# Kernel optimization log

Measured on AMD Instinct MI355X. Metric: run time of the kernel, lower is better.

The kernel has to match this reference:

```python
import jax, jax.numpy as jnp
import numpy as np

B, T, C = 2, 2048, 1024
H, D, R = 16, 64, 32  # heads, head_dim, compression rank (R < D)


def setup_inputs() -> dict:
    key = jax.random.key(0)
    ks = jax.random.split(key, 8)
    s = 0.02
    return {
        "hidden_states": jax.random.normal(ks[0], (B, T, C), jnp.float32),
        "c_attn_w": jax.random.normal(ks[1], (C, 3 * C), jnp.float32) * s,
        "c_attn_b": jnp.zeros((3 * C,), jnp.float32),
        "c_proj_w": jax.random.normal(ks[2], (C, C), jnp.float32) * s,
        "c_proj_b": jnp.zeros((C,), jnp.float32),
        "wk_c": jax.random.normal(ks[3], (D, R), jnp.float32) * (1.0 / np.sqrt(D)),
        "wk_e": jax.random.normal(ks[4], (R, D), jnp.float32) * (1.0 / np.sqrt(R)),
        "wv_c": jax.random.normal(ks[5], (D, R), jnp.float32) * (1.0 / np.sqrt(D)),
        "wv_e": jax.random.normal(ks[6], (R, D), jnp.float32) * (1.0 / np.sqrt(R)),
    }


def reference(hidden_states, c_attn_w, c_attn_b, c_proj_w, c_proj_b,
              wk_c, wk_e, wv_c, wv_e):
    b, t, c = hidden_states.shape
    # GPT2 Conv1D: x @ W + b, then split into Q, K, V
    qkv = hidden_states @ c_attn_w + c_attn_b  # [B,T,3C]
    q, k, v = jnp.split(qkv, 3, axis=-1)

    def split_heads(x):  # [B,T,C] -> [B,H,T,D]
        return x.reshape(b, t, H, D).transpose(0, 2, 1, 3)

    q = split_heads(q)
    k = split_heads(k)
    v = split_heads(v)

    # Low-rank KV compression then expansion (rank R < D path)
    k_lat = jnp.einsum('bhtd,dr->bhtr', k, wk_c)  # [B,H,T,R]
    v_lat = jnp.einsum('bhtd,dr->bhtr', v, wv_c)
    k_exp = jnp.einsum('bhtr,rd->bhtd', k_lat, wk_e)  # [B,H,T,D]
    v_exp = jnp.einsum('bhtr,rd->bhtd', v_lat, wv_e)

    # Causal SDPA (attention_mask is None and q_len > 1 -> is_causal=True)
    scale = 1.0 / np.sqrt(D).astype(np.float32)
    scores = jnp.einsum('bhqd,bhkd->bhqk', q, k_exp) * scale  # [B,H,T,T]
    causal = jnp.tril(jnp.ones((t, t), dtype=bool))
    scores = jnp.where(causal[None, None], scores, jnp.finfo(scores.dtype).min)
    probs = jax.nn.softmax(scores, axis=-1)
    attn = jnp.einsum('bhqk,bhkd->bhqd', probs, v_exp)  # [B,H,T,D]

    # Merge heads and output projection
    attn = attn.transpose(0, 2, 1, 3).reshape(b, t, c)
    out = attn @ c_proj_w + c_proj_b
    return out
```

## Files before the change

### kernel.cpp

```cpp
#include <hip/hip_runtime.h>
#include <cstddef>

typedef __attribute__((ext_vector_type(8))) __bf16 bf16x8;
typedef __attribute__((ext_vector_type(4))) float f32x4;
typedef unsigned short u16;
typedef unsigned int   u32;

#define SCLF (0.125f * 1.44269504f)

__device__ __forceinline__ u16 f2bf(float f){
  union { float f; u32 u; } v; v.f = f;
  u32 r = v.u + 0x7FFFu + ((v.u >> 16) & 1u);
  return (u16)(r >> 16);
}
__device__ __forceinline__ u32 cvtpk(float lo, float hi){
  u32 r; asm("v_cvt_pk_bf16_f32 %0, %1, %2" : "=v"(r) : "v"(lo), "v"(hi)); return r;
}
__device__ __forceinline__ void gll16(const void* g, void* l){
  __builtin_amdgcn_global_load_lds((__attribute__((address_space(1))) void*)g,
                                   (__attribute__((address_space(3))) void*)l, 16, 0, 0);
}

__global__ __launch_bounds__(256) void convert_all(const float* __restrict__ x,
      const float* __restrict__ Wa, const float* __restrict__ ba, const float* __restrict__ Wp,
      const float* __restrict__ kc, const float* __restrict__ ke,
      const float* __restrict__ vc, const float* __restrict__ ve,
      u16* __restrict__ Xb, u16* __restrict__ Wab, u16* __restrict__ Mb,
      float* __restrict__ b2, u16* __restrict__ WpTb){
  __shared__ float SH[4160];
  const int bid = blockIdx.x, tid = threadIdx.x;
  if (bid < 4096){
    int i = bid*256 + tid;
    float4 v = ((const float4*)x)[i];
    uint2 r; r.x = cvtpk(v.x, v.y); r.y = cvtpk(v.z, v.w);
    ((uint2*)Xb)[i] = r;
  } else if (bid < 7168){
    int i = (bid-4096)*256 + tid;
    float4 v = ((const float4*)Wa)[i];
    uint2 r; r.x = cvtpk(v.x, v.y); r.y = cvtpk(v.z, v.w);
    ((uint2*)Wab)[i] = r;
  } else if (bid == 7168){
    #pragma unroll
    for (int t=0;t<8;++t){
      int idx = t*256 + tid;
      Mb[idx] = f2bf(ke[idx]*SCLF);
      int d = idx>>5, r = idx&31;
      Mb[2048 + r*64 + d] = f2bf(kc[idx]);
      Mb[4096 + r*64 + d] = f2bf(vc[idx]);
      Mb[6144 + idx] = f2bf(ve[idx]);
    }
  } else if (bid < 7172){
    const int part = bid - 7169;
    float* BaL = SH;
    float* W65 = SH + 1024;
    *(float4*)&BaL[tid*4] = *(const float4*)&ba[part*1024 + tid*4];
    {
      const float* msrc = (part==0) ? ke : (part==1) ? kc : vc;
      #pragma unroll
      for (int i=0;i<8;++i){
        int idx = tid + i*256;
        float v = msrc[idx];
        int r, d;
        if (part == 0){ r = idx >> 6; d = idx & 63; }
        else          { d = idx >> 5; r = idx & 31; }
        W65[r*65 + d] = v;
      }
    }
    __syncthreads();
    const float scl = (part==0) ? SCLF : 1.f;
    #pragma unroll
    for (int t=0;t<2;++t){
      int l = tid + t*256;
      int hh = l >> 5, r = l & 31;
      float acc = 0.f;
      for (int d=0;d<64;++d) acc += BaL[hh*64 + d] * W65[r*65 + d];
      b2[part*512 + l] = acc * scl;
    }
  } else {
    const int idx2 = bid - 7172;
    const int c0 = (idx2 & 15)*64, n0 = (idx2 >> 4)*64;
    float* tile = SH;
    int tx = tid & 63, ty = tid >> 6;
    #pragma unroll 4
    for (int k=0;k<16;++k){
      int r = 4*k + ty;
      tile[r*65 + tx] = Wp[(size_t)(c0+r)*1024 + n0 + tx];
    }
    __syncthreads();
    #pragma unroll 4
    for (int k=0;k<16;++k){
      int r = 4*k + ty;
      WpTb[(size_t)(n0+r)*1024 + c0 + tx] = f2bf(tile[tx*65 + r]);
    }
  }
}

__global__ __launch_bounds__(256) void fold_gemms(const u16* __restrict__ Wab,
      const u16* __restrict__ Mb, const u16* __restrict__ WpTb,
      u16* __restrict__ Wt, u16* __restrict__ W2t){
  __shared__ u16 As[4096];
  __shared__ u16 Bs[2048];
  const int cc = blockIdx.x, y = blockIdx.y;
  const int tid = threadIdx.x, wv = tid>>6, ln = tid&63;
  const int lr = ln&15, g8 = (ln>>4)*8, gq = ln>>4;
  const int c0 = cc*64;
  const int lrow = ln>>3, lcol = ((ln&7) ^ lrow)*8;
  const int swz = (lr&7)*8;
  const bool qkv = (y < 48);
  const int ph = qkv ? y : (y - 48);
  const u16* A = qkv ? (Wab + (size_t)c0*3072 + ph*64) : (WpTb + (size_t)c0*1024 + ph*64);
  const u16* B = qkv ? (Mb + (ph>>4)*2048) : (Mb + 6144);
  const size_t astr = qkv ? 3072 : 1024;
  #pragma unroll
  for (int it=0;it<3;++it){
    int c3 = wv*3 + it;
    if (c3 < 8) gll16(A + (size_t)(c3*8+lrow)*astr + lcol, &As[c3*512]);
    else { int bc = c3-8; gll16(B + (bc*8+lrow)*64 + lcol, &Bs[bc*512]); }
  }
  __syncthreads();
  f32x4 acc[2] = {};
  const int wr = (wv>>1)*32, wn = wv&1;
  #pragma unroll
  for (int ks=0;ks<2;++ks){
    int off = (ks*32 + g8) ^ swz;
    bf16x8 bf = *(const bf16x8*)&Bs[(wn*16+lr)*64 + off];
    #pragma unroll
    for (int mt=0;mt<2;++mt){
      bf16x8 af = *(const bf16x8*)&As[(wr+mt*16+lr)*64 + off];
      acc[mt] = __builtin_amdgcn_mfma_f32_16x16x32_bf16(af, bf, acc[mt], 0,0,0);
    }
  }
  if (qkv){
    const int n = (ph>>4)*512 + (ph&15)*32 + wn*16 + lr;
    #pragma unroll
    for (int mt=0;mt<2;++mt){
      union { u16 s[4]; uint2 v; } pk;
      #pragma unroll
      for (int r=0;r<4;++r) pk.s[r] = f2bf(acc[mt][r]);
      *(uint2*)&Wt[(size_t)n*1024 + c0 + wr + mt*16 + 4*gq] = pk.v;
    }
  } else {
    const int col = ph*32 + wn*16 + lr;
    #pragma unroll
    for (int mt=0;mt<2;++mt)
      #pragma unroll
      for (int r=0;r<4;++r)
        W2t[(size_t)(c0 + wr + mt*16 + 4*gq + r)*512 + col] = f2bf(acc[mt][r]);
  }
}

template<typename OT>
__global__ __launch_bounds__(256) void gemm64(const u16* __restrict__ A, const u16* __restrict__ Bt,
        const float* __restrict__ bias, OT* __restrict__ C, u16* __restrict__ Vt,
        int M, int N, int K, int ldc){
  __shared__ u16 As[64*64];
  __shared__ u16 Bs[128*64];
  const int nwg = gridDim.x * gridDim.y;
  const int id  = blockIdx.x + gridDim.x * blockIdx.y;
  const int nid = (id & 7) * (nwg >> 3) + (id >> 3);
  const int bx = nid % gridDim.x, by = nid / gridDim.x;
  const int tid = threadIdx.x, wv = tid>>6, ln = tid&63;
  const int lr = ln&15, g8 = (ln>>4)*8;
  const int m0 = bx*64, n0 = by*128;
  const int wr = (wv>>1)*32, wc = (wv&1)*64;
  const int lrow = ln>>3, lcol = ((ln&7) ^ lrow)*8;
  const int swz = (lr&7)*8;
  f32x4 acc[2][4] = {};
  const int nk = K >> 6;
  for (int kt=0; kt<nk; ++kt){
    #pragma unroll
    for (int it=0; it<6; ++it){
      int chunk = wv*6 + it;
      if (chunk < 8){
        int row = chunk*8 + lrow;
        gll16(A + (size_t)(m0+row)*K + kt*64 + lcol, &As[chunk*512]);
      } else {
        int bc = chunk - 8;
        int row = bc*8 + lrow;
        gll16(Bt + (size_t)(n0+row)*K + kt*64 + lcol, &Bs[bc*512]);
      }
    }
    __syncthreads();
    #pragma unroll
    for (int ks=0; ks<2; ++ks){
      int off = (ks*32 + g8) ^ swz;
      bf16x8 af[2], bfr[4];
      #pragma unroll
      for (int mt=0;mt<2;++mt) af[mt]  = *(const bf16x8*)&As[(wr+mt*16+lr)*64 + off];
      #pragma unroll
      for (int nt=0;nt<4;++nt) bfr[nt] = *(const bf16x8*)&Bs[(wc+nt*16+lr)*64 + off];
      #pragma unroll
      for (int mt=0;mt<2;++mt)
        #pragma unroll
        for (int nt=0;nt<4;++nt)
          acc[mt][nt] = __builtin_amdgcn_mfma_f32_16x16x32_bf16(af[mt], bfr[nt], acc[mt][nt], 0,0,0);
    }
    __syncthreads();
  }
  if (Vt && n0 >= 1024){
    #pragma unroll
    for (int mt=0;mt<2;++mt){
      int row0 = m0 + wr + mt*16 + 4*(ln>>4);
      int tin  = row0 & 2047;
      int p0 = 4*((tin>>4)&1) + 8*((tin>>2)&3) + 32*(tin>>5);
      size_t vbase = (size_t)(row0 >> 11) * 512;
      #pragma unroll
      for (int nt=0;nt<4;++nt){
        int col = n0 + wc + nt*16 + lr;
        float bv = bias[col];
        int nlat = col - 1024;
        union { u16 s[4]; uint2 v; } pk;
        #pragma unroll
        for (int r=0;r<4;++r) pk.s[r] = f2bf(acc[mt][nt][r] + bv);
        *(uint2*)&Vt[(vbase + nlat)*2048 + p0] = pk.v;
      }
    }
  } else {
    #pragma unroll
    for (int mt=0;mt<2;++mt){
      int row = m0 + wr + mt*16 + 4*(ln>>4);
      #pragma unroll
      for (int nt=0;nt<4;++nt){
        int col = n0 + wc + nt*16 + lr;
        float bv = bias[col];
        #pragma unroll
        for (int r=0;r<4;++r){
          float v = acc[mt][nt][r] + bv;
          if constexpr (sizeof(OT) == 2) C[(size_t)(row+r)*ldc + col] = f2bf(v);
          else                           C[(size_t)(row+r)*ldc + col] = v;
        }
      }
    }
  }
}

__global__ __launch_bounds__(256, 4) void attn_fwd(const u16* __restrict__ QKV,
            const u16* __restrict__ Vt, u16* __restrict__ Out){
  const int bh = blockIdx.x;
  const int y = blockIdx.y;
  const int qt = (y < 8) ? y : (y < 16) ? 23 - y : (y < 24) ? y : 55 - y;
  const int b = bh >> 4, h = bh & 15;
  const int tid = threadIdx.x, wv = tid>>6, ln = tid&63;
  const int sg = wv>>1, wvL = wv&1;
  const int lr = ln&15, gq = ln>>4;
  __shared__ __align__(16) char SMEM[32768];
  u16* KB0 = (u16*)SMEM           + (sg*2    )*2048;
  u16* KB1 = (u16*)SMEM           + (sg*2 + 1)*2048;
  u16* VB0 = (u16*)(SMEM + 16384) + (sg*2    )*2048;
  u16* VB1 = (u16*)(SMEM + 16384) + (sg*2 + 1)*2048;
  const int q0 = qt*64;
  const size_t base = (size_t)(b*2048) * 1536;
  const u16* qrowA = QKV + base + (size_t)(q0 + wvL*32 + lr)*1536 + h*32;
  bf16x8 qfA = *(const bf16x8*)(qrowA + gq*8);
  bf16x8 qfB = *(const bf16x8*)(qrowA + (size_t)16*1536 + gq*8);
  const int qgA = q0 + wvL*32 + lr, qgB = qgA + 16;
  f32x4 oA0 = {}, oA1 = {}, oB0 = {}, oB1 = {};
  float lA = 0.f, lB = 0.f;
  const u16* ksrc = QKV + base + 512 + h*32;
  const u16* vsrc = Vt + (size_t)(bh*32)*2048;

  const int ci = wvL*64 + ln;
  const int rK = ci>>2, cK = 8*((ci&3) ^ (rK&3));
  const int rV = ci>>3, cV = 8*((ci&7) ^ (rV&7));

  int offK[4], offV[2][2];
  #pragma unroll
  for (int nt=0;nt<4;++nt)
    offK[nt] = (nt*16+lr)*64 + ((gq*16) ^ ((lr&3)<<4));
  #pragma unroll
  for (int dt=0;dt<2;++dt)
    #pragma unroll
    for (int c=0;c<2;++c)
      offV[dt][c] = (dt*16+lr)*128 + ((c*64 + gq*16) ^ ((lr&7)<<4));

  if (sg <= qt){
    gll16(ksrc + (size_t)(sg*64 + rK)*1536 + cK,      KB0 + wvL*512);
    gll16(ksrc + (size_t)(sg*64 + 32 + rK)*1536 + cK, KB0 + 1024 + wvL*512);
    gll16(vsrc + (size_t)rV*2048 + sg*64 + cV,        VB0 + wvL*512);
    gll16(vsrc + (size_t)(16+rV)*2048 + sg*64 + cV,   VB0 + 1024 + wvL*512);
  }
  __syncthreads();
  const u16* kpa = ksrc + (size_t)(sg*64 + 128 + rK)*1536 + cK;
  const u16* kpb = ksrc + (size_t)(sg*64 + 160 + rK)*1536 + cK;
  const u16* vpa = vsrc + (size_t)rV*2048 + sg*64 + 128 + cV;
  const u16* vpb = vsrc + (size_t)(16+rV)*2048 + sg*64 + 128 + cV;
  const size_t KSTEP = (size_t)128*1536;

  #define ABODY(II, KBC, VBC, KBN, VBN) do { \
    const int kt = 2*(II) + sg; \
    if (kt + 2 <= qt){ \
      gll16(kpa, (KBN) + wvL*512); \
      gll16(kpb, (KBN) + 1024 + wvL*512); \
      gll16(vpa, (VBN) + wvL*512); \
      gll16(vpb, (VBN) + 1024 + wvL*512); \
      kpa += KSTEP; kpb += KSTEP; vpa += 128; vpb += 128; \
    } \
    if (kt <= qt){ \
      f32x4 sA[4] = {}, sB[4] = {}; \
      __builtin_amdgcn_s_setprio(1); \
      _Pragma("unroll") for (int nt=0;nt<4;++nt){ \
        bf16x8 k0 = *(const bf16x8*)((const char*)(KBC) + offK[nt]); \
        sA[nt] = __builtin_amdgcn_mfma_f32_16x16x32_bf16(k0, qfA, sA[nt], 0,0,0); \
        sB[nt] = __builtin_amdgcn_mfma_f32_16x16x32_bf16(k0, qfB, sB[nt], 0,0,0); \
      } \
      __builtin_amdgcn_s_setprio(0); \
      if (kt == qt){ \
        const int kv0 = kt*64; \
        _Pragma("unroll") for (int nt=0;nt<4;++nt) \
        _Pragma("unroll") for (int r=0;r<4;++r){ \
          int k = kv0 + nt*16 + 4*gq + r; \
          if (k > qgA) sA[nt][r] = -1e30f; \
          if (k > qgB) sB[nt][r] = -1e30f; \
        } \
      } \
      union { u32 u[4]; bf16x8 v; } paA0, paA1, paB0, paB1; \
      { \
        float p0,p1,p2,p3,p4,p5,p6,p7; \
        p0=__builtin_amdgcn_exp2f(sA[0][0]); p1=__builtin_amdgcn_exp2f(sA[0][1]); \
        p2=__builtin_amdgcn_exp2f(sA[0][2]); p3=__builtin_amdgcn_exp2f(sA[0][3]); \
        p4=__builtin_amdgcn_exp2f(sA[1][0]); p5=__builtin_amdgcn_exp2f(sA[1][1]); \
        p6=__builtin_amdgcn_exp2f(sA[1][2]); p7=__builtin_amdgcn_exp2f(sA[1][3]); \
        lA += ((p0+p1)+(p2+p3)) + ((p4+p5)+(p6+p7)); \
        paA0.u[0]=cvtpk(p0,p1); paA0.u[1]=cvtpk(p2,p3); paA0.u[2]=cvtpk(p4,p5); paA0.u[3]=cvtpk(p6,p7); \
        p0=__builtin_amdgcn_exp2f(sA[2][0]); p1=__builtin_amdgcn_exp2f(sA[2][1]); \
        p2=__builtin_amdgcn_exp2f(sA[2][2]); p3=__builtin_amdgcn_exp2f(sA[2][3]); \
        p4=__builtin_amdgcn_exp2f(sA[3][0]); p5=__builtin_amdgcn_exp2f(sA[3][1]); \
        p6=__builtin_amdgcn_exp2f(sA[3][2]); p7=__builtin_amdgcn_exp2f(sA[3][3]); \
        lA += ((p0+p1)+(p2+p3)) + ((p4+p5)+(p6+p7)); \
        paA1.u[0]=cvtpk(p0,p1); paA1.u[1]=cvtpk(p2,p3); paA1.u[2]=cvtpk(p4,p5); paA1.u[3]=cvtpk(p6,p7); \
        p0=__builtin_amdgcn_exp2f(sB[0][0]); p1=__builtin_amdgcn_exp2f(sB[0][1]); \
        p2=__builtin_amdgcn_exp2f(sB[0][2]); p3=__builtin_amdgcn_exp2f(sB[0][3]); \
        p4=__builtin_amdgcn_exp2f(sB[1][0]); p5=__builtin_amdgcn_exp2f(sB[1][1]); \
        p6=__builtin_amdgcn_exp2f(sB[1][2]); p7=__builtin_amdgcn_exp2f(sB[1][3]); \
        lB += ((p0+p1)+(p2+p3)) + ((p4+p5)+(p6+p7)); \
        paB0.u[0]=cvtpk(p0,p1); paB0.u[1]=cvtpk(p2,p3); paB0.u[2]=cvtpk(p4,p5); paB0.u[3]=cvtpk(p6,p7); \
        p0=__builtin_amdgcn_exp2f(sB[2][0]); p1=__builtin_amdgcn_exp2f(sB[2][1]); \
        p2=__builtin_amdgcn_exp2f(sB[2][2]); p3=__builtin_amdgcn_exp2f(sB[2][3]); \
        p4=__builtin_amdgcn_exp2f(sB[3][0]); p5=__builtin_amdgcn_exp2f(sB[3][1]); \
        p6=__builtin_amdgcn_exp2f(sB[3][2]); p7=__builtin_amdgcn_exp2f(sB[3][3]); \
        lB += ((p0+p1)+(p2+p3)) + ((p4+p5)+(p6+p7)); \
        paB1.u[0]=cvtpk(p0,p1); paB1.u[1]=cvtpk(p2,p3); paB1.u[2]=cvtpk(p4,p5); paB1.u[3]=cvtpk(p6,p7); \
      } \
      __builtin_amdgcn_s_setprio(1); \
      { \
        bf16x8 v00 = *(const bf16x8*)((const char*)(VBC) + offV[0][0]); \
        bf16x8 v10 = *(const bf16x8*)((const char*)(VBC) + offV[1][0]); \
        bf16x8 v01 = *(const bf16x8*)((const char*)(VBC) + offV[0][1]); \
        bf16x8 v11 = *(const bf16x8*)((const char*)(VBC) + offV[1][1]); \
        oA0 = __builtin_amdgcn_mfma_f32_16x16x32_bf16(paA0.v, v00, oA0, 0,0,0); \
        oA1 = __builtin_amdgcn_mfma_f32_16x16x32_bf16(paA0.v, v10, oA1, 0,0,0); \
        oB0 = __builtin_amdgcn_mfma_f32_16x16x32_bf16(paB0.v, v00, oB0, 0,0,0); \
        oB1 = __builtin_amdgcn_mfma_f32_16x16x32_bf16(paB0.v, v10, oB1, 0,0,0); \
        oA0 = __builtin_amdgcn_mfma_f32_16x16x32_bf16(paA1.v, v01, oA0, 0,0,0); \
        oA1 = __builtin_amdgcn_mfma_f32_16x16x32_bf16(paA1.v, v11, oA1, 0,0,0); \
        oB0 = __builtin_amdgcn_mfma_f32_16x16x32_bf16(paB1.v, v01, oB0, 0,0,0); \
        oB1 = __builtin_amdgcn_mfma_f32_16x16x32_bf16(paB1.v, v11, oB1, 0,0,0); \
      } \
      __builtin_amdgcn_s_setprio(0); \
    } \
    __syncthreads(); \
  } while(0)

  const int nmax = (qt + 2) >> 1;
  const int jmax = (nmax + 1) >> 1;
  for (int j = 0; j < jmax; ++j){
    ABODY(2*j,   KB0, VB0, KB1, VB1);
    ABODY(2*j+1, KB1, VB1, KB0, VB0);
  }
  lA += __shfl_xor(lA, 16); lA += __shfl_xor(lA, 32);
  lB += __shfl_xor(lB, 16); lB += __shfl_xor(lB, 32);

  float* MO = (float*)SMEM;
  float* ML = (float*)(SMEM + 12288);
  if (sg == 1){
    #pragma unroll
    for (int r=0;r<4;++r){
      int rowA = wvL*32 + 4*gq + r;
      MO[rowA*34 + lr]            = oA0[r];
      MO[rowA*34 + 16 + lr]       = oA1[r];
      MO[(rowA+16)*34 + lr]       = oB0[r];
      MO[(rowA+16)*34 + 16 + lr]  = oB1[r];
    }
    if (gq == 0){ ML[wvL*32 + lr] = lA; ML[wvL*32 + 16 + lr] = lB; }
  }
  __syncthreads();
  if (sg == 0){
    float lSA = lA + ML[wvL*32 + lr];
    float lSB = lB + ML[wvL*32 + 16 + lr];
    float lA_o[4], lB_o[4];
    #pragma unroll
    for (int r=0;r<4;++r){ lA_o[r] = __shfl(lSA, 4*gq + r); lB_o[r] = __shfl(lSB, 4*gq + r); }
    #pragma unroll
    for (int r=0;r<4;++r){
      int rowA = wvL*32 + 4*gq + r;
      float vA0 = (oA0[r] + MO[rowA*34 + lr])           / lA_o[r];
      float vA1 = (oA1[r] + MO[rowA*34 + 16 + lr])      / lA_o[r];
      float vB0 = (oB0[r] + MO[(rowA+16)*34 + lr])      / lB_o[r];
      float vB1 = (oB1[r] + MO[(rowA+16)*34 + 16 + lr]) / lB_o[r];
      size_t obA = (size_t)(b*2048 + q0 + rowA)*512 + h*32;
      Out[obA + lr]      = f2bf(vA0);
      Out[obA + 16 + lr] = f2bf(vA1);
      size_t obB = obA + (size_t)16*512;
      Out[obB + lr]      = f2bf(vB0);
      Out[obB + 16 + lr] = f2bf(vB1);
    }
  }
}

#define WS_B2   0u
#define WS_WT   8192u
#define WS_W2T  (WS_WT + 3145728u)
#define WS_XB   (WS_W2T + 1048576u)
#define WS_QKV  (WS_XB + 8388608u)
#define WS_VT   (WS_QKV + 12582912u)
#define WS_ATT  (WS_VT + 4194304u)
#define WS_WAB  (WS_ATT + 4194304u)
#define WS_WPT  (WS_WAB + 6291456u)
#define WS_MB   (WS_WPT + 2097152u)

extern "C" void kernel_launch(void* const* d_in, const int* in_sizes, int n_in,
                              void* d_out, int out_size, void* d_ws, size_t ws_size,
                              hipStream_t stream) {
  const float* x  = (const float*)d_in[0];
  const float* Wa = (const float*)d_in[1];
  const float* ba = (const float*)d_in[2];
  const float* Wp = (const float*)d_in[3];
  const float* bp = (const float*)d_in[4];
  const float* kc = (const float*)d_in[5];
  const float* ke = (const float*)d_in[6];
  const float* vc = (const float*)d_in[7];
  const float* ve = (const float*)d_in[8];
  float* out = (float*)d_out;
  char* ws = (char*)d_ws;
  float* b2  = (float*)(ws + WS_B2);
  u16* Wt    = (u16*)(ws + WS_WT);
  u16* W2t   = (u16*)(ws + WS_W2T);
  u16* Xb    = (u16*)(ws + WS_XB);
  u16* QKVb  = (u16*)(ws + WS_QKV);
  u16* Vt    = (u16*)(ws + WS_VT);
  u16* Att   = (u16*)(ws + WS_ATT);
  u16* Wab   = (u16*)(ws + WS_WAB);
  u16* WpTb  = (u16*)(ws + WS_WPT);
  u16* Mb    = (u16*)(ws + WS_MB);

  convert_all<<<7428, 256, 0, stream>>>(x, Wa, ba, Wp, kc, ke, vc, ve, Xb, Wab, Mb, b2, WpTb);
  fold_gemms<<<dim3(16,64), 256, 0, stream>>>(Wab, Mb, WpTb, Wt, W2t);
  gemm64<u16><<<dim3(64,12), 256, 0, stream>>>(Xb, Wt, b2, QKVb, Vt, 4096, 1536, 1024, 1536);
  attn_fwd<<<dim3(32,32), 256, 0, stream>>>(QKVb, Vt, Att);
  gemm64<float><<<dim3(64,8), 256, 0, stream>>>(Att, W2t, bp, out, (u16*)nullptr, 4096, 1024, 512, 1024);
}
```

Before: 73.42 us.

## Fuse weight conversion into fold GEMMs and load GEMM A-operand directly to registers

Merges the convert and fold kernels into one prep kernel in which fold blocks read fp32 weights directly, convert them to bf16 in shared memory and run the small MFMA fold. This drops the intermediate bf16 copies of Wa, Wp-transpose and the small matrices, along with one kernel launch. Separately, the main GEMM now loads A fragments straight from global memory into registers instead of staging them through LDS, which halves LDS traffic but relies on uncoalesced per-lane 16-byte global loads. The Wp transpose now goes through a padded fp32 shared tile inside the fold block.

```diff
diff --git a/kernel.cpp b/kernel.cpp
--- a/kernel.cpp
+++ b/kernel.cpp
@@ -21,36 +21,27 @@
                                    (__attribute__((address_space(3))) void*)l, 16, 0, 0);
 }
 
-__global__ __launch_bounds__(256) void convert_all(const float* __restrict__ x,
+__global__ __launch_bounds__(256) void prep_fused(const float* __restrict__ x,
       const float* __restrict__ Wa, const float* __restrict__ ba, const float* __restrict__ Wp,
       const float* __restrict__ kc, const float* __restrict__ ke,
       const float* __restrict__ vc, const float* __restrict__ ve,
-      u16* __restrict__ Xb, u16* __restrict__ Wab, u16* __restrict__ Mb,
-      float* __restrict__ b2, u16* __restrict__ WpTb){
-  __shared__ float SH[4160];
+      u16* __restrict__ Xb, float* __restrict__ b2,
+      u16* __restrict__ Wt, u16* __restrict__ W2t){
+  __shared__ __align__(16) char PS[28928];
+  float* SH = (float*)PS;
+  u16* As = (u16*)(PS + 16640);
+  u16* Bs = (u16*)(PS + 16640 + 8192);
   const int bid = blockIdx.x, tid = threadIdx.x;
+
   if (bid < 4096){
     int i = bid*256 + tid;
     float4 v = ((const float4*)x)[i];
     uint2 r; r.x = cvtpk(v.x, v.y); r.y = cvtpk(v.z, v.w);
     ((uint2*)Xb)[i] = r;
-  } else if (bid < 7168){
-    int i = (bid-4096)*256 + tid;
-    float4 v = ((const float4*)Wa)[i];
-    uint2 r; r.x = cvtpk(v.x, v.y); r.y = cvtpk(v.z, v.w);
-    ((uint2*)Wab)[i] = r;
-  } else if (bid == 7168){
-    #pragma unroll
-    for (int t=0;t<8;++t){
-      int idx = t*256 + tid;
-      Mb[idx] = f2bf(ke[idx]*SCLF);
-      int d = idx>>5, r = idx&31;
-      Mb[2048 + r*64 + d] = f2bf(kc[idx]);
-      Mb[4096 + r*64 + d] = f2bf(vc[idx]);
-      Mb[6144 + idx] = f2bf(ve[idx]);
-    }
-  } else if (bid < 7172){
-    const int part = bid - 7169;
+    return;
+  }
+  if (bid < 4099){
+    const int part = bid - 4096;
     float* BaL = SH;
     float* W65 = SH + 1024;
     *(float4*)&BaL[tid*4] = *(const float4*)&ba[part*1024 + tid*4];
@@ -76,62 +67,55 @@
       for (int d=0;d<64;++d) acc += BaL[hh*64 + d] * W65[r*65 + d];
       b2[part*512 + l] = acc * scl;
     }
-  } else {
-    const int idx2 = bid - 7172;
-    const int c0 = (idx2 & 15)*64, n0 = (idx2 >> 4)*64;
-    float* tile = SH;
-    int tx = tid & 63, ty = tid >> 6;
-    #pragma unroll 4
-    for (int k=0;k<16;++k){
-      int r = 4*k + ty;
-      tile[r*65 + tx] = Wp[(size_t)(c0+r)*1024 + n0 + tx];
-    }
-    __syncthreads();
-    #pragma unroll 4
-    for (int k=0;k<16;++k){
-      int r = 4*k + ty;
-      WpTb[(size_t)(n0+r)*1024 + c0 + tx] = f2bf(tile[tx*65 + r]);
-    }
-  }
-}
-
-__global__ __launch_bounds__(256) void fold_gemms(const u16* __restrict__ Wab,
-      const u16* __restrict__ Mb, const u16* __restrict__ WpTb,
-      u16* __restrict__ Wt, u16* __restrict__ W2t){
-  __shared__ u16 As[4096];
-  __shared__ u16 Bs[2048];
-  const int cc = blockIdx.x, y = blockIdx.y;
-  const int tid = threadIdx.x, wv = tid>>6, ln = tid&63;
+    return;
+  }
+
+  const int wv = tid>>6, ln = tid&63;
   const int lr = ln&15, g8 = (ln>>4)*8, gq = ln>>4;
-  const int c0 = cc*64;
-  const int lrow = ln>>3, lcol = ((ln&7) ^ lrow)*8;
   const int swz = (lr&7)*8;
-  const bool qkv = (y < 48);
-  const int ph = qkv ? y : (y - 48);
-  const u16* A = qkv ? (Wab + (size_t)c0*3072 + ph*64) : (WpTb + (size_t)c0*1024 + ph*64);
-  const u16* B = qkv ? (Mb + (ph>>4)*2048) : (Mb + 6144);
-  const size_t astr = qkv ? 3072 : 1024;
-  #pragma unroll
-  for (int it=0;it<3;++it){
-    int c3 = wv*3 + it;
-    if (c3 < 8) gll16(A + (size_t)(c3*8+lrow)*astr + lcol, &As[c3*512]);
-    else { int bc = c3-8; gll16(B + (bc*8+lrow)*64 + lcol, &Bs[bc*512]); }
-  }
-  __syncthreads();
-  f32x4 acc[2] = {};
-  const int wr = (wv>>1)*32, wn = wv&1;
-  #pragma unroll
-  for (int ks=0;ks<2;++ks){
-    int off = (ks*32 + g8) ^ swz;
-    bf16x8 bf = *(const bf16x8*)&Bs[(wn*16+lr)*64 + off];
-    #pragma unroll
-    for (int mt=0;mt<2;++mt){
-      bf16x8 af = *(const bf16x8*)&As[(wr+mt*16+lr)*64 + off];
-      acc[mt] = __builtin_amdgcn_mfma_f32_16x16x32_bf16(af, bf, acc[mt], 0,0,0);
-    }
-  }
-  if (qkv){
-    const int n = (ph>>4)*512 + (ph&15)*32 + wn*16 + lr;
+
+  if (bid < 4867){
+    const int f = bid - 4099;
+    const int cc = f & 15, ph = f >> 4;
+    const int part = ph >> 4;
+    const int c0 = cc*64;
+    {
+      int r = tid>>3, d8 = tid&7;
+      float v[8];
+      if (part == 0){
+        #pragma unroll
+        for (int j=0;j<8;++j) v[j] = ke[r*64 + d8*8 + j]*SCLF;
+      } else {
+        const float* m = (part==1) ? kc : vc;
+        #pragma unroll
+        for (int j=0;j<8;++j) v[j] = m[(d8*8+j)*32 + r];
+      }
+      uint4 w; w.x=cvtpk(v[0],v[1]); w.y=cvtpk(v[2],v[3]); w.z=cvtpk(v[4],v[5]); w.w=cvtpk(v[6],v[7]);
+      *(uint4*)&Bs[r*64 + ((d8 ^ (r&7))*8)] = w;
+    }
+    #pragma unroll
+    for (int p=0;p<2;++p){
+      int g2 = p*256 + tid;
+      int row = g2>>3, gcol = g2&7;
+      const float* src = Wa + (size_t)(c0+row)*3072 + ph*64 + gcol*8;
+      float4 a = ((const float4*)src)[0], b = ((const float4*)src)[1];
+      uint4 w; w.x=cvtpk(a.x,a.y); w.y=cvtpk(a.z,a.w); w.z=cvtpk(b.x,b.y); w.w=cvtpk(b.z,b.w);
+      *(uint4*)&As[row*64 + ((gcol ^ (row&7))*8)] = w;
+    }
+    __syncthreads();
+    f32x4 acc[2] = {};
+    const int wr = (wv>>1)*32, wn = wv&1;
+    #pragma unroll
+    for (int ks=0;ks<2;++ks){
+      int off = (ks*32 + g8) ^ swz;
+      bf16x8 bf = *(const bf16x8*)&Bs[(wn*16+lr)*64 + off];
+      #pragma unroll
+      for (int mt=0;mt<2;++mt){
+        bf16x8 af = *(const bf16x8*)&As[(wr+mt*16+lr)*64 + off];
+        acc[mt] = __builtin_amdgcn_mfma_f32_16x16x32_bf16(af, bf, acc[mt], 0,0,0);
+      }
+    }
+    const int n = part*512 + (ph&15)*32 + wn*16 + lr;
     #pragma unroll
     for (int mt=0;mt<2;++mt){
       union { u16 s[4]; uint2 v; } pk;
@@ -140,6 +124,52 @@
       *(uint2*)&Wt[(size_t)n*1024 + c0 + wr + mt*16 + 4*gq] = pk.v;
     }
   } else {
+    const int f = bid - 4867;
+    const int cc = f & 15, ph = f >> 4;
+    const int c0 = cc*64;
+    {
+      int r = tid>>2, c4 = (tid&3)*16;
+      const float* src = Wp + (size_t)(ph*64 + r)*1024 + c0 + c4;
+      float4 v0 = ((const float4*)src)[0], v1 = ((const float4*)src)[1],
+             v2 = ((const float4*)src)[2], v3 = ((const float4*)src)[3];
+      float* dst = &SH[r*65 + c4];
+      dst[0]=v0.x; dst[1]=v0.y; dst[2]=v0.z; dst[3]=v0.w;
+      dst[4]=v1.x; dst[5]=v1.y; dst[6]=v1.z; dst[7]=v1.w;
+      dst[8]=v2.x; dst[9]=v2.y; dst[10]=v2.z; dst[11]=v2.w;
+      dst[12]=v3.x; dst[13]=v3.y; dst[14]=v3.z; dst[15]=v3.w;
+    }
+    {
+      int r = tid>>3, d8 = tid&7;
+      float v[8];
+      #pragma unroll
+      for (int j=0;j<8;++j) v[j] = ve[r*64 + d8*8 + j];
+      uint4 w; w.x=cvtpk(v[0],v[1]); w.y=cvtpk(v[2],v[3]); w.z=cvtpk(v[4],v[5]); w.w=cvtpk(v[6],v[7]);
+      *(uint4*)&Bs[r*64 + ((d8 ^ (r&7))*8)] = w;
+    }
+    __syncthreads();
+    #pragma unroll
+    for (int p=0;p<2;++p){
+      int g2 = p*256 + tid;
+      int j = g2>>3, d8 = g2&7;
+      float v[8];
+      #pragma unroll
+      for (int jj=0;jj<8;++jj) v[jj] = SH[(d8*8+jj)*65 + j];
+      uint4 w; w.x=cvtpk(v[0],v[1]); w.y=cvtpk(v[2],v[3]); w.z=cvtpk(v[4],v[5]); w.w=cvtpk(v[6],v[7]);
+      *(uint4*)&As[j*64 + ((d8 ^ (j&7))*8)] = w;
+    }
+    __syncthreads();
+    f32x4 acc[2] = {};
+    const int wr = (wv>>1)*32, wn = wv&1;
+    #pragma unroll
+    for (int ks=0;ks<2;++ks){
+      int off = (ks*32 + g8) ^ swz;
+      bf16x8 bf = *(const bf16x8*)&Bs[(wn*16+lr)*64 + off];
+      #pragma unroll
+      for (int mt=0;mt<2;++mt){
+        bf16x8 af = *(const bf16x8*)&As[(wr+mt*16+lr)*64 + off];
+        acc[mt] = __builtin_amdgcn_mfma_f32_16x16x32_bf16(af, bf, acc[mt], 0,0,0);
+      }
+    }
     const int col = ph*32 + wn*16 + lr;
     #pragma unroll
     for (int mt=0;mt<2;++mt)
@@ -153,47 +183,45 @@
 __global__ __launch_bounds__(256) void gemm64(const u16* __restrict__ A, const u16* __restrict__ Bt,
         const float* __restrict__ bias, OT* __restrict__ C, u16* __restrict__ Vt,
         int M, int N, int K, int ldc){
-  __shared__ u16 As[64*64];
   __shared__ u16 Bs[128*64];
   const int nwg = gridDim.x * gridDim.y;
   const int id  = blockIdx.x + gridDim.x * blockIdx.y;
   const int nid = (id & 7) * (nwg >> 3) + (id >> 3);
   const int bx = nid % gridDim.x, by = nid / gridDim.x;
   const int tid = threadIdx.x, wv = tid>>6, ln = tid&63;
-  const int lr = ln&15, g8 = (ln>>4)*8;
+  const int lr = ln&15, g8 = (ln>>4)*8, gq = ln>>4;
   const int m0 = bx*64, n0 = by*128;
   const int wr = (wv>>1)*32, wc = (wv&1)*64;
   const int lrow = ln>>3, lcol = ((ln&7) ^ lrow)*8;
   const int swz = (lr&7)*8;
+  const u16* aptr = A + (size_t)(m0 + wr + lr)*K + gq*8;
   f32x4 acc[2][4] = {};
   const int nk = K >> 6;
   for (int kt=0; kt<nk; ++kt){
     #pragma unroll
-    for (int it=0; it<6; ++it){
-      int chunk = wv*6 + it;
-      if (chunk < 8){
-        int row = chunk*8 + lrow;
-        gll16(A + (size_t)(m0+row)*K + kt*64 + lcol, &As[chunk*512]);
-      } else {
-        int bc = chunk - 8;
-        int row = bc*8 + lrow;
-        gll16(Bt + (size_t)(n0+row)*K + kt*64 + lcol, &Bs[bc*512]);
-      }
-    }
+    for (int it=0; it<4; ++it){
+      int bc = wv*4 + it;
+      int row = bc*8 + lrow;
+      gll16(Bt + (size_t)(n0+row)*K + kt*64 + lcol, &Bs[bc*512]);
+    }
+    bf16x8 aF[2][2];
+    #pragma unroll
+    for (int mt=0;mt<2;++mt)
+      #pragma unroll
+      for (int ks=0;ks<2;++ks)
+        aF[mt][ks] = *(const bf16x8*)(aptr + (size_t)(mt*16)*K + kt*64 + ks*32);
     __syncthreads();
     #pragma unroll
     for (int ks=0; ks<2; ++ks){
       int off = (ks*32 + g8) ^ swz;
-      bf16x8 af[2], bfr[4];
-      #pragma unroll
-      for (int mt=0;mt<2;++mt) af[mt]  = *(const bf16x8*)&As[(wr+mt*16+lr)*64 + off];
+      bf16x8 bfr[4];
       #pragma unroll
       for (int nt=0;nt<4;++nt) bfr[nt] = *(const bf16x8*)&Bs[(wc+nt*16+lr)*64 + off];
       #pragma unroll
       for (int mt=0;mt<2;++mt)
         #pragma unroll
         for (int nt=0;nt<4;++nt)
-          acc[mt][nt] = __builtin_amdgcn_mfma_f32_16x16x32_bf16(af[mt], bfr[nt], acc[mt][nt], 0,0,0);
+          acc[mt][nt] = __builtin_amdgcn_mfma_f32_16x16x32_bf16(aF[mt][ks], bfr[nt], acc[mt][nt], 0,0,0);
     }
     __syncthreads();
   }
@@ -414,9 +442,6 @@
 #define WS_QKV  (WS_XB + 8388608u)
 #define WS_VT   (WS_QKV + 12582912u)
 #define WS_ATT  (WS_VT + 4194304u)
-#define WS_WAB  (WS_ATT + 4194304u)
-#define WS_WPT  (WS_WAB + 6291456u)
-#define WS_MB   (WS_WPT + 2097152u)
 
 extern "C" void kernel_launch(void* const* d_in, const int* in_sizes, int n_in,
                               void* d_out, int out_size, void* d_ws, size_t ws_size,
@@ -439,12 +464,8 @@
   u16* QKVb  = (u16*)(ws + WS_QKV);
   u16* Vt    = (u16*)(ws + WS_VT);
   u16* Att   = (u16*)(ws + WS_ATT);
-  u16* Wab   = (u16*)(ws + WS_WAB);
-  u16* WpTb  = (u16*)(ws + WS_WPT);
-  u16* Mb    = (u16*)(ws + WS_MB);
-
-  convert_all<<<7428, 256, 0, stream>>>(x, Wa, ba, Wp, kc, ke, vc, ve, Xb, Wab, Mb, b2, WpTb);
-  fold_gemms<<<dim3(16,64), 256, 0, stream>>>(Wab, Mb, WpTb, Wt, W2t);
+
+  prep_fused<<<5123, 256, 0, stream>>>(x, Wa, ba, Wp, kc, ke, vc, ve, Xb, b2, Wt, W2t);
   gemm64<u16><<<dim3(64,12), 256, 0, stream>>>(Xb, Wt, b2, QKVb, Vt, 4096, 1536, 1024, 1536);
   attn_fwd<<<dim3(32,32), 256, 0, stream>>>(QKVb, Vt, Att);
   gemm64<float><<<dim3(64,8), 256, 0, stream>>>(Att, W2t, bp, out, (u16*)nullptr, 4096, 1024, 512, 1024);
```

Result: slower. 83.01 us (+13.1%).
